# Optimization experiments

Measured on AMD Instinct MI355X. Metric: run time of the kernel, lower is better.

## Reference

```python
import jax, jax.numpy as jnp
import numpy as np

DIM = 1024
HEADS = 16
DIM_HEAD = 64
EPS = 1e-5


def setup_inputs() -> dict:
    key = jax.random.key(0)
    ks = jax.random.split(key, 8)
    s = 1.0 / np.sqrt(DIM)
    return {
        "x": jax.random.normal(ks[0], (4, 2048, DIM), dtype=jnp.float32),
        "ln_w": jnp.ones((DIM,), jnp.float32),
        "ln_b": jnp.zeros((DIM,), jnp.float32),
        "wq": jax.random.normal(ks[1], (DIM, DIM), jnp.float32) * s,
        "bq": jax.random.normal(ks[2], (DIM,), jnp.float32) * s,
        "wk": jax.random.normal(ks[3], (DIM, DIM), jnp.float32) * s,
        "bk": jax.random.normal(ks[4], (DIM,), jnp.float32) * s,
        "wv": jax.random.normal(ks[5], (DIM, DIM), jnp.float32) * s,
        "bv": jax.random.normal(ks[6], (DIM,), jnp.float32) * s,
    }


def _split_heads(t):
    b, n, _ = t.shape
    return t.reshape(b, n, HEADS, DIM_HEAD).transpose(0, 2, 1, 3)  # b h n d


def reference(x, ln_w, ln_b, wq, bq, wk, bk, wv, bv):
    # LayerNorm over last dim
    mu = jnp.mean(x, axis=-1, keepdims=True)
    var = jnp.mean(jnp.square(x - mu), axis=-1, keepdims=True)
    h = (x - mu) * jax.lax.rsqrt(var + EPS) * ln_w + ln_b

    q = _split_heads(h @ wq + bq)
    k = _split_heads(h @ wk + bk)
    v = _split_heads(h @ wv + bv)

    scale = 1.0 / jnp.sqrt(jnp.float32(DIM_HEAD))
    scores = jnp.einsum('bhnd,bhmd->bhnm', q, k) * scale
    att = jax.nn.softmax(scores, axis=-1)
    out = jnp.einsum('bhnm,bhmd->bhnd', att, v)
    b, _, n, _ = out.shape
    return out.transpose(0, 2, 1, 3).reshape(b, n, HEADS * DIM_HEAD)
```

## Files before the change

### kernel.cpp

```cpp
#include <hip/hip_runtime.h>
#include <hip/hip_bf16.h>
#include <stdint.h>

#define DIM    1024
#define HEADS  16
#define DHEAD  64
#define SEQ    2048
#define BATCH  4

typedef unsigned short u16;
typedef __attribute__((ext_vector_type(4))) float f32x4;
typedef __attribute__((ext_vector_type(8))) short bf16x8;

#define QSCALE 0.18033688011112042f

__device__ inline u16 f2bf(float f) {
  __hip_bfloat16 h = __float2bfloat16(f);
  return *reinterpret_cast<u16*>(&h);
}

__device__ inline uint32_t pack_bf16_rhu(float lo, float hi) {
  uint32_t a = __float_as_uint(lo) + 0x8000u;
  uint32_t b = __float_as_uint(hi) + 0x8000u;
  return (b & 0xFFFF0000u) | (a >> 16);
}

__device__ inline void async_load16(const void* g, void* l) {
  __builtin_amdgcn_global_load_lds((const __attribute__((address_space(1))) void*)g,
                                   (__attribute__((address_space(3))) void*)l, 16, 0, 0);
}

__global__ __launch_bounds__(256) void ln_kernel(const float* __restrict__ x,
                                                 const float* __restrict__ w,
                                                 const float* __restrict__ b,
                                                 u16* __restrict__ h) {
  int row = blockIdx.x;
  int t = threadIdx.x;
  const float4* xr = (const float4*)(x + (size_t)row * DIM);
  float4 v = xr[t];
  float s  = v.x + v.y + v.z + v.w;
  float s2 = v.x*v.x + v.y*v.y + v.z*v.z + v.w*v.w;
  for (int m = 1; m < 64; m <<= 1) { s += __shfl_xor(s, m); s2 += __shfl_xor(s2, m); }
  __shared__ float ss[4], ss2[4];
  int wid = t >> 6;
  if ((t & 63) == 0) { ss[wid] = s; ss2[wid] = s2; }
  __syncthreads();
  s  = ss[0] + ss[1] + ss[2] + ss[3];
  s2 = ss2[0] + ss2[1] + ss2[2] + ss2[3];
  float mu  = s * (1.0f / DIM);
  float var = s2 * (1.0f / DIM) - mu * mu;
  float rs  = rsqrtf(var + 1e-5f);
  float4 wv4 = ((const float4*)w)[t];
  float4 bv4 = ((const float4*)b)[t];
  ushort4 o;
  o.x = f2bf((v.x - mu) * rs * wv4.x + bv4.x);
  o.y = f2bf((v.y - mu) * rs * wv4.y + bv4.y);
  o.z = f2bf((v.z - mu) * rs * wv4.z + bv4.z);
  o.w = f2bf((v.w - mu) * rs * wv4.w + bv4.w);
  ((ushort4*)(h + (size_t)row * DIM))[t] = o;
}

__global__ __launch_bounds__(256) void wt_kernel(const float* __restrict__ wq,
                                                 const float* __restrict__ wk,
                                                 const float* __restrict__ wv,
                                                 u16* __restrict__ wt) {
  int mat = blockIdx.z;
  const float* w = (mat == 0) ? wq : ((mat == 1) ? wk : wv);
  __shared__ float tile[32][33];
  int j0 = blockIdx.x * 32, d0 = blockIdx.y * 32;
  int tc = threadIdx.x & 31, tr = threadIdx.x >> 5;
  for (int i = 0; i < 32; i += 8)
    tile[tr + i][tc] = w[(size_t)(d0 + tr + i) * DIM + j0 + tc];
  __syncthreads();
  u16* dst = wt + (size_t)mat * DIM * DIM;
  for (int i = 0; i < 32; i += 8)
    dst[(size_t)(j0 + tr + i) * DIM + d0 + tc] = f2bf(tile[tc][tr + i]);
}

__global__ __launch_bounds__(256, 2) void gemm_qkv(const u16* __restrict__ A,
                                                   const u16* __restrict__ Bt,
                                                   const float* __restrict__ bq,
                                                   const float* __restrict__ bk,
                                                   const float* __restrict__ bv,
                                                   u16* __restrict__ qo,
                                                   u16* __restrict__ ko,
                                                   u16* __restrict__ vo) {
  __shared__ u16 smem[2 * 12288];
  int t = threadIdx.x;
  int bm = blockIdx.x, bn = blockIdx.y;
  const u16* Ab = A + (size_t)bm * 128 * DIM;
  const u16* Bb = Bt + (size_t)bn * 256 * DIM;
  int lane = t & 63, w = t >> 6;
  int wm = (w >> 1) * 64, wn = (w & 1) * 128;
  int fr = lane & 15;
  int quad = lane >> 4;
  f32x4 acc[4][8];
  for (int i = 0; i < 4; ++i) for (int j = 0; j < 8; ++j) acc[i][j] = (f32x4)(0.0f);

  {
    u16* lA = smem; u16* lB = smem + 4096;
#pragma unroll
    for (int r = 0; r < 2; ++r) {
      int flat = (t + r * 256) * 8;
      int m = flat >> 5, c = (flat >> 3) & 3;
      async_load16(Ab + (size_t)m * DIM + ((c ^ (m & 3)) << 3), lA + flat);
    }
#pragma unroll
    for (int r = 0; r < 4; ++r) {
      int flat = (t + r * 256) * 8;
      int m = flat >> 5, c = (flat >> 3) & 3;
      async_load16(Bb + (size_t)m * DIM + ((c ^ (m & 3)) << 3), lB + flat);
    }
  }

  for (int it = 0; it < 32; ++it) {
    __syncthreads();
    if (it < 31) {
      int k0 = (it + 1) * 32;
      u16* lA = smem + ((it + 1) & 1) * 12288;
      u16* lB = lA + 4096;
#pragma unroll
      for (int r = 0; r < 2; ++r) {
        int flat = (t + r * 256) * 8;
        int m = flat >> 5, c = (flat >> 3) & 3;
        async_load16(Ab + (size_t)m * DIM + k0 + ((c ^ (m & 3)) << 3), lA + flat);
      }
#pragma unroll
      for (int r = 0; r < 4; ++r) {
        int flat = (t + r * 256) * 8;
        int m = flat >> 5, c = (flat >> 3) & 3;
        async_load16(Bb + (size_t)m * DIM + k0 + ((c ^ (m & 3)) << 3), lB + flat);
      }
    }
    const u16* lA = smem + (it & 1) * 12288;
    const u16* lB = lA + 4096;
    bf16x8 af[4], bfm[8];
#pragma unroll
    for (int i = 0; i < 4; ++i) {
      int m = wm + i * 16 + fr;
      af[i] = *(const bf16x8*)(lA + m * 32 + ((quad ^ (m & 3)) << 3));
    }
#pragma unroll
    for (int j = 0; j < 8; ++j) {
      int m = wn + j * 16 + fr;
      bfm[j] = *(const bf16x8*)(lB + m * 32 + ((quad ^ (m & 3)) << 3));
    }
#pragma unroll
    for (int i = 0; i < 4; ++i)
#pragma unroll
      for (int j = 0; j < 8; ++j)
        acc[i][j] = __builtin_amdgcn_mfma_f32_16x16x32_bf16(af[i], bfm[j], acc[i][j], 0, 0, 0);
  }

  int matu = bn >> 2;
  int b = bm >> 4;
  int nb = (bm & 15) * 128 + wm + quad * 4;
  if (matu == 0) {
#pragma unroll
    for (int j = 0; j < 8; ++j) {
      int c = (bn * 256 + wn + j * 16 + fr) & 1023;
      float bb = bq[c];
      int head = c >> 6, d = c & 63;
      u16* base = qo + (size_t)(b * HEADS + head) * SEQ * DHEAD + d;
#pragma unroll
      for (int i = 0; i < 4; ++i)
#pragma unroll
        for (int r = 0; r < 4; ++r) {
          int n = nb + i * 16 + r;
          base[(size_t)n * DHEAD] = f2bf((acc[i][j][r] + bb) * QSCALE);
        }
    }
  } else if (matu == 1) {
#pragma unroll
    for (int j = 0; j < 8; ++j) {
      int c = (bn * 256 + wn + j * 16 + fr) & 1023;
      float bb = bk[c];
      int head = c >> 6, d = c & 63;
      u16* base = ko + (size_t)(b * HEADS + head) * SEQ * DHEAD + (d & 7);
      int dc = d >> 3;
#pragma unroll
      for (int i = 0; i < 4; ++i)
#pragma unroll
        for (int r = 0; r < 4; ++r) {
          int n = nb + i * 16 + r;
          base[(size_t)(n >> 7) * 8192 + (size_t)(n & 127) * 64
               + ((dc ^ (n & 7)) << 3)] = f2bf(acc[i][j][r] + bb);
        }
    }
  } else {
    float bbj[8]; int dj[8]; size_t hbj[8];
#pragma unroll
    for (int j = 0; j < 8; ++j) {
      int c = (bn * 256 + wn + j * 16 + fr) & 1023;
      bbj[j] = bv[c];
      dj[j] = c & 63;
      hbj[j] = (size_t)(b * HEADS + (c >> 6)) * SEQ * DHEAD;
    }
#pragma unroll
    for (int i = 0; i < 4; ++i) {
      int n0 = nb + i * 16;
      int n127 = n0 & 127; int kv5 = n127 & 31;
      int s0 = (n127 & 96) | ((kv5 & 12) << 1) | ((kv5 & 16) >> 2);
      size_t ro = (size_t)(n0 >> 7) * 8192 + (s0 & 7);
      int sc = s0 >> 3;
#pragma unroll
      for (int j = 0; j < 8; ++j) {
        uint2 pv;
        pv.x = pack_bf16_rhu(acc[i][j][0] + bbj[j], acc[i][j][1] + bbj[j]);
        pv.y = pack_bf16_rhu(acc[i][j][2] + bbj[j], acc[i][j][3] + bbj[j]);
        *(uint2*)(vo + hbj[j] + ro + (size_t)dj[j] * 128 + ((sc ^ (dj[j] & 15)) << 3)) = pv;
      }
    }
  }
}

__global__ __launch_bounds__(256, 2) void flash_attn(const u16* __restrict__ Q,
                                                     const u16* __restrict__ Ksw,
                                                     const u16* __restrict__ Vsw,
                                                     float* __restrict__ out) {
  __shared__ __align__(16) u16 smem[2 * 16384];

  int t = threadIdx.x;
  int lane = t & 63, w = t >> 6;
  int wrow = w * 32;
  int fr = lane & 15, quad = lane >> 4, fk = quad * 8;
  int qtile = blockIdx.x, bh = blockIdx.y;
  int b = bh >> 4, head = bh & 15;

  const u16* Qb  = Q   + ((size_t)bh * SEQ + qtile * 128) * DHEAD;
  const u16* Kbh = Ksw + (size_t)bh * SEQ * DHEAD;
  const u16* Vbh = Vsw + (size_t)bh * SEQ * DHEAD;

  for (int p = 0; p < 4; ++p) {
    int flat = (t + p * 256) * 8;
    async_load16(Qb + flat, smem + flat);
  }
  __syncthreads();
  bf16x8 aq[2][2];
  for (int mi = 0; mi < 2; ++mi)
    for (int ks = 0; ks < 2; ++ks)
      aq[mi][ks] = *(const bf16x8*)(smem + (wrow + mi * 16 + fr) * 64 + ks * 32 + fk);
  __syncthreads();

  for (int p = 0; p < 4; ++p) {
    int flat = (t + p * 256) * 8;
    async_load16(Kbh + flat, smem + flat);
    async_load16(Vbh + flat, smem + 8192 + flat);
  }

  const f32x4 Z = (f32x4)(0.0f);
  f32x4 O[4][2];
  for (int nd = 0; nd < 4; ++nd) for (int mi = 0; mi < 2; ++mi) O[nd][mi] = Z;
  float lsum[2] = {0.0f, 0.0f};

  for (int it = 0; it < 16; ++it) {
    __syncthreads();
    if (it < 15) {
      u16* dst = smem + ((it + 1) & 1) * 16384;
      const u16* Kb = Kbh + (size_t)(it + 1) * 8192;
      const u16* Vb = Vbh + (size_t)(it + 1) * 8192;
#pragma unroll
      for (int p = 0; p < 4; ++p) {
        int flat = (t + p * 256) * 8;
        async_load16(Kb + flat, dst + flat);
        async_load16(Vb + flat, dst + 8192 + flat);
      }
    }
    const u16* lK  = smem + (it & 1) * 16384;
    const u16* lVt = lK + 8192;

    f32x4 T[8][2];
#pragma unroll
    for (int ni = 0; ni < 8; ++ni) {
      int kv = ni * 16 + fr;
      int sw = kv & 7;
      bf16x8 kb0 = *(const bf16x8*)(lK + kv * 64 + ((quad ^ sw) << 3));
      bf16x8 kb1 = *(const bf16x8*)(lK + kv * 64 + (((4 + quad) ^ sw) << 3));
      T[ni][0] = __builtin_amdgcn_mfma_f32_16x16x32_bf16(kb0, aq[0][0], Z, 0, 0, 0);
      T[ni][0] = __builtin_amdgcn_mfma_f32_16x16x32_bf16(kb1, aq[0][1], T[ni][0], 0, 0, 0);
      T[ni][1] = __builtin_amdgcn_mfma_f32_16x16x32_bf16(kb0, aq[1][0], Z, 0, 0, 0);
      T[ni][1] = __builtin_amdgcn_mfma_f32_16x16x32_bf16(kb1, aq[1][1], T[ni][1], 0, 0, 0);
    }

    uint32_t pkA[8][2], pkB[8][2];
#pragma unroll
    for (int mi = 0; mi < 2; ++mi) {
      float s = 0.0f;
#pragma unroll
      for (int ni = 0; ni < 8; ++ni) {
        float p0 = __builtin_amdgcn_exp2f(T[ni][mi][0]);
        float p1 = __builtin_amdgcn_exp2f(T[ni][mi][1]);
        float p2 = __builtin_amdgcn_exp2f(T[ni][mi][2]);
        float p3 = __builtin_amdgcn_exp2f(T[ni][mi][3]);
        s += (p0 + p1) + (p2 + p3);
        pkA[ni][mi] = pack_bf16_rhu(p0, p1);
        pkB[ni][mi] = pack_bf16_rhu(p2, p3);
      }
      lsum[mi] += s;
    }

#pragma unroll
    for (int ks = 0; ks < 4; ++ks) {
      bf16x8 pa[2];
#pragma unroll
      for (int mi = 0; mi < 2; ++mi) {
        union { uint32_t u[4]; bf16x8 v; } cvt;
        cvt.u[0] = pkA[2 * ks][mi];
        cvt.u[1] = pkB[2 * ks][mi];
        cvt.u[2] = pkA[2 * ks + 1][mi];
        cvt.u[3] = pkB[2 * ks + 1][mi];
        pa[mi] = cvt.v;
      }
#pragma unroll
      for (int nd = 0; nd < 4; ++nd) {
        int d = nd * 16 + fr;
        bf16x8 vb = *(const bf16x8*)(lVt + d * 128 + (((ks * 4 + quad) ^ (d & 15)) << 3));
        O[nd][0] = __builtin_amdgcn_mfma_f32_16x16x32_bf16(vb, pa[0], O[nd][0], 0, 0, 0);
        O[nd][1] = __builtin_amdgcn_mfma_f32_16x16x32_bf16(vb, pa[1], O[nd][1], 0, 0, 0);
      }
    }
  }

  float* ob = out + ((size_t)b * SEQ + qtile * 128) * DIM + head * DHEAD;
#pragma unroll
  for (int mi = 0; mi < 2; ++mi) {
    float ls = lsum[mi];
    ls += __shfl_xor(ls, 16);
    ls += __shfl_xor(ls, 32);
    float inv = 1.0f / ls;
    int q = wrow + mi * 16 + fr;
#pragma unroll
    for (int nd = 0; nd < 4; ++nd) {
      float4 vv;
      vv.x = O[nd][mi][0] * inv;
      vv.y = O[nd][mi][1] * inv;
      vv.z = O[nd][mi][2] * inv;
      vv.w = O[nd][mi][3] * inv;
      *(float4*)(ob + (size_t)q * DIM + nd * 16 + quad * 4) = vv;
    }
  }
}

extern "C" void kernel_launch(void* const* d_in, const int* in_sizes, int n_in,
                              void* d_out, int out_size, void* d_ws, size_t ws_size,
                              hipStream_t stream) {
  const float* x   = (const float*)d_in[0];
  const float* lnw = (const float*)d_in[1];
  const float* lnb = (const float*)d_in[2];
  const float* wq  = (const float*)d_in[3];
  const float* bq  = (const float*)d_in[4];
  const float* wk  = (const float*)d_in[5];
  const float* bk  = (const float*)d_in[6];
  const float* wv  = (const float*)d_in[7];
  const float* bv  = (const float*)d_in[8];
  float* out = (float*)d_out;

  char* ws = (char*)d_ws;
  u16* h  = (u16*)(ws);
  u16* wt = (u16*)(ws + 16777216);
  u16* q  = (u16*)(ws + 23068672);
  u16* k  = (u16*)(ws + 39845888);
  u16* v  = (u16*)(ws + 56623104);

  ln_kernel<<<8192, 256, 0, stream>>>(x, lnw, lnb, h);
  wt_kernel<<<dim3(32, 32, 3), 256, 0, stream>>>(wq, wk, wv, wt);
  gemm_qkv<<<dim3(64, 12), 256, 0, stream>>>(h, wt, bq, bk, bv, q, k, v);
  flash_attn<<<dim3(16, 64), 256, 0, stream>>>(q, k, v, out);
}
```

Measured before the change: 244.6 us.

## Widen attention blocks, compute row sums via MFMA, single-buffer GEMM with BK=64

```diff
diff --git a/kernel.cpp b/kernel.cpp
--- a/kernel.cpp
+++ b/kernel.cpp
@@ -85,7 +85,8 @@
                                                    u16* __restrict__ qo,
                                                    u16* __restrict__ ko,
                                                    u16* __restrict__ vo) {
-  __shared__ u16 smem[2 * 12288];
+  __shared__ u16 lA[128 * 64];
+  __shared__ u16 lB[256 * 64];
   int t = threadIdx.x;
   int bm = blockIdx.x, bn = blockIdx.y;
   const u16* Ab = A + (size_t)bm * 128 * DIM;
@@ -97,59 +98,42 @@
   f32x4 acc[4][8];
   for (int i = 0; i < 4; ++i) for (int j = 0; j < 8; ++j) acc[i][j] = (f32x4)(0.0f);
 
-  {
-    u16* lA = smem; u16* lB = smem + 4096;
-#pragma unroll
-    for (int r = 0; r < 2; ++r) {
-      int flat = (t + r * 256) * 8;
-      int m = flat >> 5, c = (flat >> 3) & 3;
-      async_load16(Ab + (size_t)m * DIM + ((c ^ (m & 3)) << 3), lA + flat);
-    }
+  for (int k0 = 0; k0 < DIM; k0 += 64) {
+    __syncthreads();
 #pragma unroll
     for (int r = 0; r < 4; ++r) {
       int flat = (t + r * 256) * 8;
-      int m = flat >> 5, c = (flat >> 3) & 3;
-      async_load16(Bb + (size_t)m * DIM + ((c ^ (m & 3)) << 3), lB + flat);
-    }
-  }
-
-  for (int it = 0; it < 32; ++it) {
+      int m = flat >> 6, c = (flat >> 3) & 7;
+      int gk = k0 + ((c ^ (m & 7)) << 3);
+      async_load16(Ab + (size_t)m * DIM + gk, lA + flat);
+    }
+#pragma unroll
+    for (int r = 0; r < 8; ++r) {
+      int flat = (t + r * 256) * 8;
+      int m = flat >> 6, c = (flat >> 3) & 7;
+      int gk = k0 + ((c ^ (m & 7)) << 3);
+      async_load16(Bb + (size_t)m * DIM + gk, lB + flat);
+    }
     __syncthreads();
-    if (it < 31) {
-      int k0 = (it + 1) * 32;
-      u16* lA = smem + ((it + 1) & 1) * 12288;
-      u16* lB = lA + 4096;
-#pragma unroll
-      for (int r = 0; r < 2; ++r) {
-        int flat = (t + r * 256) * 8;
-        int m = flat >> 5, c = (flat >> 3) & 3;
-        async_load16(Ab + (size_t)m * DIM + k0 + ((c ^ (m & 3)) << 3), lA + flat);
-      }
-#pragma unroll
-      for (int r = 0; r < 4; ++r) {
-        int flat = (t + r * 256) * 8;
-        int m = flat >> 5, c = (flat >> 3) & 3;
-        async_load16(Bb + (size_t)m * DIM + k0 + ((c ^ (m & 3)) << 3), lB + flat);
-      }
-    }
-    const u16* lA = smem + (it & 1) * 12288;
-    const u16* lB = lA + 4096;
-    bf16x8 af[4], bfm[8];
-#pragma unroll
-    for (int i = 0; i < 4; ++i) {
-      int m = wm + i * 16 + fr;
-      af[i] = *(const bf16x8*)(lA + m * 32 + ((quad ^ (m & 3)) << 3));
-    }
-#pragma unroll
-    for (int j = 0; j < 8; ++j) {
-      int m = wn + j * 16 + fr;
-      bfm[j] = *(const bf16x8*)(lB + m * 32 + ((quad ^ (m & 3)) << 3));
-    }
-#pragma unroll
-    for (int i = 0; i < 4; ++i)
-#pragma unroll
-      for (int j = 0; j < 8; ++j)
-        acc[i][j] = __builtin_amdgcn_mfma_f32_16x16x32_bf16(af[i], bfm[j], acc[i][j], 0, 0, 0);
+#pragma unroll
+    for (int ks = 0; ks < 2; ++ks) {
+      bf16x8 af[4], bfm[8];
+#pragma unroll
+      for (int i = 0; i < 4; ++i) {
+        int m = wm + i * 16 + fr;
+        af[i] = *(const bf16x8*)(lA + m * 64 + (((ks * 4 + quad) ^ (m & 7)) << 3));
+      }
+#pragma unroll
+      for (int j = 0; j < 8; ++j) {
+        int m = wn + j * 16 + fr;
+        bfm[j] = *(const bf16x8*)(lB + m * 64 + (((ks * 4 + quad) ^ (m & 7)) << 3));
+      }
+#pragma unroll
+      for (int i = 0; i < 4; ++i)
+#pragma unroll
+        for (int j = 0; j < 8; ++j)
+          acc[i][j] = __builtin_amdgcn_mfma_f32_16x16x32_bf16(af[i], bfm[j], acc[i][j], 0, 0, 0);
+    }
   }
 
   int matu = bn >> 2;
@@ -214,7 +198,7 @@
   }
 }
 
-__global__ __launch_bounds__(256, 2) void flash_attn(const u16* __restrict__ Q,
+__global__ __launch_bounds__(512, 4) void flash_attn(const u16* __restrict__ Q,
                                                      const u16* __restrict__ Ksw,
                                                      const u16* __restrict__ Vsw,
                                                      float* __restrict__ out) {
@@ -227,12 +211,12 @@
   int qtile = blockIdx.x, bh = blockIdx.y;
   int b = bh >> 4, head = bh & 15;
 
-  const u16* Qb  = Q   + ((size_t)bh * SEQ + qtile * 128) * DHEAD;
+  const u16* Qb  = Q   + ((size_t)bh * SEQ + qtile * 256) * DHEAD;
   const u16* Kbh = Ksw + (size_t)bh * SEQ * DHEAD;
   const u16* Vbh = Vsw + (size_t)bh * SEQ * DHEAD;
 
   for (int p = 0; p < 4; ++p) {
-    int flat = (t + p * 256) * 8;
+    int flat = (t + p * 512) * 8;
     async_load16(Qb + flat, smem + flat);
   }
   __syncthreads();
@@ -242,16 +226,18 @@
       aq[mi][ks] = *(const bf16x8*)(smem + (wrow + mi * 16 + fr) * 64 + ks * 32 + fk);
   __syncthreads();
 
-  for (int p = 0; p < 4; ++p) {
-    int flat = (t + p * 256) * 8;
+  for (int p = 0; p < 2; ++p) {
+    int flat = (t + p * 512) * 8;
     async_load16(Kbh + flat, smem + flat);
     async_load16(Vbh + flat, smem + 8192 + flat);
   }
 
   const f32x4 Z = (f32x4)(0.0f);
+  const bf16x8 ones = (bf16x8)((short)0x3F80);
   f32x4 O[4][2];
   for (int nd = 0; nd < 4; ++nd) for (int mi = 0; mi < 2; ++mi) O[nd][mi] = Z;
-  float lsum[2] = {0.0f, 0.0f};
+  f32x4 Lacc[2];
+  Lacc[0] = Z; Lacc[1] = Z;
 
   for (int it = 0; it < 16; ++it) {
     __syncthreads();
@@ -260,8 +246,8 @@
       const u16* Kb = Kbh + (size_t)(it + 1) * 8192;
       const u16* Vb = Vbh + (size_t)(it + 1) * 8192;
 #pragma unroll
-      for (int p = 0; p < 4; ++p) {
-        int flat = (t + p * 256) * 8;
+      for (int p = 0; p < 2; ++p) {
+        int flat = (t + p * 512) * 8;
         async_load16(Kb + flat, dst + flat);
         async_load16(Vb + flat, dst + 8192 + flat);
       }
@@ -285,18 +271,15 @@
     uint32_t pkA[8][2], pkB[8][2];
 #pragma unroll
     for (int mi = 0; mi < 2; ++mi) {
-      float s = 0.0f;
 #pragma unroll
       for (int ni = 0; ni < 8; ++ni) {
         float p0 = __builtin_amdgcn_exp2f(T[ni][mi][0]);
         float p1 = __builtin_amdgcn_exp2f(T[ni][mi][1]);
         float p2 = __builtin_amdgcn_exp2f(T[ni][mi][2]);
         float p3 = __builtin_amdgcn_exp2f(T[ni][mi][3]);
-        s += (p0 + p1) + (p2 + p3);
         pkA[ni][mi] = pack_bf16_rhu(p0, p1);
         pkB[ni][mi] = pack_bf16_rhu(p2, p3);
       }
-      lsum[mi] += s;
     }
 
 #pragma unroll
@@ -311,6 +294,8 @@
         cvt.u[3] = pkB[2 * ks + 1][mi];
         pa[mi] = cvt.v;
       }
+      Lacc[0] = __builtin_amdgcn_mfma_f32_16x16x32_bf16(ones, pa[0], Lacc[0], 0, 0, 0);
+      Lacc[1] = __builtin_amdgcn_mfma_f32_16x16x32_bf16(ones, pa[1], Lacc[1], 0, 0, 0);
 #pragma unroll
       for (int nd = 0; nd < 4; ++nd) {
         int d = nd * 16 + fr;
@@ -321,13 +306,10 @@
     }
   }
 
-  float* ob = out + ((size_t)b * SEQ + qtile * 128) * DIM + head * DHEAD;
+  float* ob = out + ((size_t)b * SEQ + qtile * 256) * DIM + head * DHEAD;
 #pragma unroll
   for (int mi = 0; mi < 2; ++mi) {
-    float ls = lsum[mi];
-    ls += __shfl_xor(ls, 16);
-    ls += __shfl_xor(ls, 32);
-    float inv = 1.0f / ls;
+    float inv = 1.0f / Lacc[mi][0];
     int q = wrow + mi * 16 + fr;
 #pragma unroll
     for (int nd = 0; nd < 4; ++nd) {
@@ -365,5 +347,5 @@
   ln_kernel<<<8192, 256, 0, stream>>>(x, lnw, lnb, h);
   wt_kernel<<<dim3(32, 32, 3), 256, 0, stream>>>(wq, wk, wv, wt);
   gemm_qkv<<<dim3(64, 12), 256, 0, stream>>>(h, wt, bq, bk, bv, q, k, v);
-  flash_attn<<<dim3(16, 64), 256, 0, stream>>>(q, k, v, out);
-}
+  flash_attn<<<dim3(8, 64), 512, 0, stream>>>(q, k, v, out);
+}
```

Measured after the change: 342.0 us. 39.8% more time.
